# Kernel optimization log

Hardware: AMD Instinct MI355X
Metric: run time of the kernel (lower is better)

## Reference

```python
import jax, jax.numpy as jnp
import numpy as np
from jax import lax

SEQ, BATCH, D_IN, HID = 2048, 16, 512, 512


def _qrnn_dir(X, W, b):
    # X: [S, B, D]; W: [3H, D]; b: [3H]
    g = jnp.einsum('sbd,hd->sbh', X, W) + b            # [S, B, 3H]
    z, f, o = jnp.split(g, 3, axis=-1)
    z = jnp.tanh(z)
    f = jax.nn.sigmoid(f)
    o = jax.nn.sigmoid(o)
    # fo-pooling recurrence: h_t = f_t*z_t + (1-f_t)*h_{t-1}, h_0 = 0
    # linear recurrence h_t = a_t*h_{t-1} + c_t with a = 1-f, c = f*z
    a = 1.0 - f
    c = f * z

    def combine(e1, e2):
        a1, c1 = e1
        a2, c2 = e2
        return (a1 * a2, a2 * c1 + c2)

    _, h = lax.associative_scan(combine, (a, c), axis=0)
    return o * h                                        # [S, B, H]


def setup_inputs() -> dict:
    key = jax.random.key(0)
    k = jax.random.split(key, 5)
    scale = 0.02
    return {
        'X': jax.random.normal(k[0], (SEQ, BATCH, D_IN), dtype=jnp.float32),
        'W_fw': jax.random.normal(k[1], (3 * HID, D_IN), dtype=jnp.float32) * scale,
        'b_fw': jnp.zeros((3 * HID,), dtype=jnp.float32),
        'W_bw': jax.random.normal(k[2], (3 * HID, D_IN), dtype=jnp.float32) * scale,
        'b_bw': jnp.zeros((3 * HID,), dtype=jnp.float32),
    }


def reference(X, W_fw, b_fw, W_bw, b_bw):
    Yfw = _qrnn_dir(X, W_fw, b_fw)                       # [S, B, H]
    Ybw = _qrnn_dir(jnp.flip(X, axis=0), W_bw, b_bw)     # [S, B, H]
    return jnp.concatenate((Yfw, jnp.flip(Ybw, axis=0)), axis=2)  # [S, B, 2H]
```

## Files before the change

kernel.cpp:

```cpp
#include <hip/hip_runtime.h>
#include <hip/hip_bf16.h>

#define SEQ   2048
#define BATCH 16
#define DIN   512
#define HID   512
#define MROWS (SEQ*BATCH)
#define NCOLS (6*HID)
#define KDIM  DIN

#define NC   64
#define CL   32
#define NSEQ (2*BATCH*HID)

typedef unsigned short u16;
typedef __bf16 bf16x8 __attribute__((ext_vector_type(8)));
typedef float  f32x4  __attribute__((ext_vector_type(4)));

__device__ __forceinline__ u16 f2bf(float x) {
  unsigned u = __float_as_uint(x);
  unsigned r = (u + 0x7fffu + ((u >> 16) & 1u)) >> 16;
  return (u16)r;
}
__device__ __forceinline__ float bflo(unsigned u) { return __uint_as_float(u << 16); }
__device__ __forceinline__ float bfhi(unsigned u) { return __uint_as_float(u & 0xffff0000u); }

__device__ __forceinline__ void async_ld16(const void* g, void* l) {
  __builtin_amdgcn_global_load_lds(
      (const __attribute__((address_space(1))) void*)g,
      (__attribute__((address_space(3))) void*)l, 16, 0, 0);
}

__device__ __forceinline__ float sig_fast(float x) {
  return __builtin_amdgcn_rcpf(1.f + __expf(-x));
}
__device__ __forceinline__ float tanh_fast(float x) {
  return 1.f - 2.f * __builtin_amdgcn_rcpf(1.f + __expf(2.f * x));
}

__global__ void cvt_kernel(const float* __restrict__ in, u16* __restrict__ out, int n4) {
  int i = blockIdx.x * blockDim.x + threadIdx.x;
  if (i >= n4) return;
  const float4 v = ((const float4*)in)[i];
  uint2 r;
  r.x = (unsigned)f2bf(v.x) | ((unsigned)f2bf(v.y) << 16);
  r.y = (unsigned)f2bf(v.z) | ((unsigned)f2bf(v.w) << 16);
  ((uint2*)out)[i] = r;
}

__launch_bounds__(256)
__global__ void gemm_gates(const u16* __restrict__ A, const u16* __restrict__ B,
                           const float* __restrict__ bfw, const float* __restrict__ bbw,
                           u16* __restrict__ G)
{
  __shared__ u16 sA[128 * 64];
  __shared__ u16 sB[128 * 64];

  const int t    = threadIdx.x;
  const int wave = t >> 6;
  const int lane = t & 63;
  const int m0 = blockIdx.y * 128;
  const int n0 = blockIdx.x * 128;
  const int wm = (wave >> 1) * 64;
  const int wn = (wave & 1) * 64;

  f32x4 acc[4][4] = {};

  const int rloc = lane >> 3;
  const int gch  = (lane & 7) ^ rloc;
  const u16* gA = A + (size_t)(m0 + wave * 32 + rloc) * KDIM + gch * 8;
  const u16* gB = B + (size_t)(n0 + wave * 32 + rloc) * KDIM + gch * 8;

  const int lm  = lane & 15;
  const int q   = lane >> 4;
  const int xs  = lm & 7;

  for (int kt = 0; kt < KDIM; kt += 64) {
    __syncthreads();
#pragma unroll
    for (int j = 0; j < 4; j++) {
      async_ld16(gA + kt + (size_t)(j * 8) * KDIM, sA + (wave * 32 + j * 8) * 64);
      async_ld16(gB + kt + (size_t)(j * 8) * KDIM, sB + (wave * 32 + j * 8) * 64);
    }
    __syncthreads();

#pragma unroll
    for (int s = 0; s < 2; s++) {
      const int cofs = ((s * 4 + q) ^ xs) * 8;
      bf16x8 af[4], bfr[4];
#pragma unroll
      for (int mi = 0; mi < 4; mi++)
        af[mi] = *(const bf16x8*)(sA + (wm + mi * 16 + lm) * 64 + cofs);
#pragma unroll
      for (int ni = 0; ni < 4; ni++)
        bfr[ni] = *(const bf16x8*)(sB + (wn + ni * 16 + lm) * 64 + cofs);
#pragma unroll
      for (int mi = 0; mi < 4; mi++)
#pragma unroll
        for (int ni = 0; ni < 4; ni++)
          acc[mi][ni] = __builtin_amdgcn_mfma_f32_16x16x32_bf16(bfr[ni], af[mi], acc[mi][ni], 0, 0, 0);
    }
  }

  const int q4 = q * 4;
#pragma unroll
  for (int ni = 0; ni < 4; ni++) {
    const int colb = n0 + wn + ni * 16 + q4;
    const int dir  = colb >= 1536 ? 1 : 0;
    const int rem  = colb - dir * 1536;
    const int gate = rem >> 9;
    const int hb   = rem & 511;
    const float4 bias4 = *(const float4*)((dir ? bbw : bfw) + rem);
    u16* Gs = G + (size_t)(dir * 3 + gate) * MROWS * HID + hb;
#pragma unroll
    for (int mi = 0; mi < 4; mi++) {
      const int m = m0 + wm + mi * 16 + lm;
      float v0 = acc[mi][ni][0] + bias4.x;
      float v1 = acc[mi][ni][1] + bias4.y;
      float v2 = acc[mi][ni][2] + bias4.z;
      float v3 = acc[mi][ni][3] + bias4.w;
      if (gate == 0) {
        v0 = tanh_fast(v0); v1 = tanh_fast(v1); v2 = tanh_fast(v2); v3 = tanh_fast(v3);
      } else {
        v0 = sig_fast(v0); v1 = sig_fast(v1); v2 = sig_fast(v2); v3 = sig_fast(v3);
      }
      uint2 pk;
      pk.x = (unsigned)f2bf(v0) | ((unsigned)f2bf(v1) << 16);
      pk.y = (unsigned)f2bf(v2) | ((unsigned)f2bf(v3) << 16);
      *(uint2*)(Gs + (size_t)m * HID) = pk;
    }
  }
}

__global__ void scan_stage1(const u16* __restrict__ G, float* __restrict__ AC) {
  const int tid = blockIdx.x * 256 + threadIdx.x;
  const int h     = (tid & 127) * 4;
  const int chunk = (tid >> 7) & 63;
  const int b     = (tid >> 13) & 15;
  const int dir   = tid >> 17;
  const u16* Zp = G + (size_t)(dir * 3 + 0) * MROWS * HID;
  const u16* Fp = G + (size_t)(dir * 3 + 1) * MROWS * HID;
  float A0 = 1.f, A1 = 1.f, A2 = 1.f, A3 = 1.f;
  float C0 = 0.f, C1 = 0.f, C2 = 0.f, C3 = 0.f;
  const int tbase = chunk * CL;
#pragma unroll 8
  for (int i = 0; i < CL; i++) {
    const int ts = tbase + i;
    const int s = dir ? (SEQ - 1 - ts) : ts;
    const size_t off = ((size_t)s * BATCH + b) * HID + h;
    const uint2 zu = *(const uint2*)(Zp + off);
    const uint2 fu = *(const uint2*)(Fp + off);
    const float z0 = bflo(zu.x), z1 = bfhi(zu.x), z2 = bflo(zu.y), z3 = bfhi(zu.y);
    const float f0 = bflo(fu.x), f1 = bfhi(fu.x), f2 = bflo(fu.y), f3 = bfhi(fu.y);
    const float a0 = 1.f - f0, a1 = 1.f - f1, a2 = 1.f - f2, a3 = 1.f - f3;
    C0 = fmaf(a0, C0, f0 * z0); A0 *= a0;
    C1 = fmaf(a1, C1, f1 * z1); A1 *= a1;
    C2 = fmaf(a2, C2, f2 * z2); A2 *= a2;
    C3 = fmaf(a3, C3, f3 * z3); A3 *= a3;
  }
  const int sidx = (dir * BATCH + b) * HID + h;
  *(float4*)&AC[(size_t)chunk * (2 * NSEQ) + sidx]        = make_float4(A0, A1, A2, A3);
  *(float4*)&AC[(size_t)chunk * (2 * NSEQ) + NSEQ + sidx] = make_float4(C0, C1, C2, C3);
}

__global__ void scan_stage2(const float* __restrict__ AC, float* __restrict__ Hin) {
  const int sidx = blockIdx.x * 256 + threadIdx.x;
  float carry = 0.f;
  for (int chunk = 0; chunk < NC; chunk++) {
    Hin[(size_t)chunk * NSEQ + sidx] = carry;
    const float Aa = AC[(size_t)chunk * (2 * NSEQ) + sidx];
    const float Cc = AC[(size_t)chunk * (2 * NSEQ) + NSEQ + sidx];
    carry = fmaf(Aa, carry, Cc);
  }
}

__global__ void scan_stage3(const u16* __restrict__ G, const float* __restrict__ Hin,
                            float* __restrict__ out) {
  const int tid = blockIdx.x * 256 + threadIdx.x;
  const int h     = (tid & 127) * 4;
  const int chunk = (tid >> 7) & 63;
  const int b     = (tid >> 13) & 15;
  const int dir   = tid >> 17;
  const u16* Zp = G + (size_t)(dir * 3 + 0) * MROWS * HID;
  const u16* Fp = G + (size_t)(dir * 3 + 1) * MROWS * HID;
  const u16* Op = G + (size_t)(dir * 3 + 2) * MROWS * HID;
  const int sidx = (dir * BATCH + b) * HID + h;
  float4 hv = *(const float4*)&Hin[(size_t)chunk * NSEQ + sidx];
  const int tbase = chunk * CL;
#pragma unroll 8
  for (int i = 0; i < CL; i++) {
    const int ts = tbase + i;
    const int s = dir ? (SEQ - 1 - ts) : ts;
    const size_t off = ((size_t)s * BATCH + b) * HID + h;
    const uint2 zu = *(const uint2*)(Zp + off);
    const uint2 fu = *(const uint2*)(Fp + off);
    const uint2 ou = *(const uint2*)(Op + off);
    const float z0 = bflo(zu.x), z1 = bfhi(zu.x), z2 = bflo(zu.y), z3 = bfhi(zu.y);
    const float f0 = bflo(fu.x), f1 = bfhi(fu.x), f2 = bflo(fu.y), f3 = bfhi(fu.y);
    hv.x = fmaf(f0, z0 - hv.x, hv.x);
    hv.y = fmaf(f1, z1 - hv.y, hv.y);
    hv.z = fmaf(f2, z2 - hv.z, hv.z);
    hv.w = fmaf(f3, z3 - hv.w, hv.w);
    f32x4 ov;
    ov[0] = bflo(ou.x) * hv.x;
    ov[1] = bfhi(ou.x) * hv.y;
    ov[2] = bflo(ou.y) * hv.z;
    ov[3] = bfhi(ou.y) * hv.w;
    __builtin_nontemporal_store(ov,
        (f32x4*)&out[((size_t)s * BATCH + b) * (2 * HID) + (size_t)dir * HID + h]);
  }
}

extern "C" void kernel_launch(void* const* d_in, const int* in_sizes, int n_in,
                              void* d_out, int out_size, void* d_ws, size_t ws_size,
                              hipStream_t stream) {
  const float* X   = (const float*)d_in[0];
  const float* Wfw = (const float*)d_in[1];
  const float* bfw = (const float*)d_in[2];
  const float* Wbw = (const float*)d_in[3];
  const float* bbw = (const float*)d_in[4];
  float* out = (float*)d_out;

  char* ws = (char*)d_ws;
  u16*   Xb  = (u16*)ws;
  u16*   Wb  = (u16*)(ws + (size_t)MROWS * KDIM * 2);
  u16*   G   = (u16*)(ws + (size_t)MROWS * KDIM * 2 + (size_t)NCOLS * KDIM * 2);
  float* AC  = (float*)((char*)G + (size_t)6 * MROWS * HID * 2);
  float* Hin = (float*)((char*)AC + (size_t)NC * 2 * NSEQ * 4);

  cvt_kernel<<<(MROWS * KDIM / 4) / 256, 256, 0, stream>>>(X, Xb, MROWS * KDIM / 4);
  cvt_kernel<<<(3 * HID * KDIM / 4) / 256, 256, 0, stream>>>(Wfw, Wb, 3 * HID * KDIM / 4);
  cvt_kernel<<<(3 * HID * KDIM / 4) / 256, 256, 0, stream>>>(Wbw, Wb + (size_t)3 * HID * KDIM,
                                                             3 * HID * KDIM / 4);

  dim3 gg(NCOLS / 128, MROWS / 128);
  gemm_gates<<<gg, 256, 0, stream>>>(Xb, Wb, bfw, bbw, G);

  scan_stage1<<<(NSEQ * NC / 4) / 256, 256, 0, stream>>>(G, AC);
  scan_stage2<<<NSEQ / 256, 256, 0, stream>>>(AC, Hin);
  scan_stage3<<<(NSEQ * NC / 4) / 256, 256, 0, stream>>>(G, Hin, out);
}
```

Measured before the change: 402.2 us.

## Fuse gate activations and intra-chunk scan into GEMM epilogue

The GEMM tile now covers the z, f and o columns for one hidden slice and one direction, so each block can apply the activations and run a local chunked linear scan over its 128 rows in registers. Partial results cross between waves through LDS. The epilogue writes compact U = o*h_local and V = o*prod(a) arrays in fp16 plus per-chunk carry data. This drops the separate stage-1 scan pass and the six-gate bf16 intermediate. The output pass becomes a single FMA per element using the combined carry. The trade-off is a longer sequential carry combine over 256 chunks, a heavier GEMM epilogue with more accumulator registers, and fp16 storage whose range and precision may differ from the reference.

```diff
diff --git a/kernel.cpp b/kernel.cpp
--- a/kernel.cpp
+++ b/kernel.cpp
@@ -1,16 +1,15 @@
 #include <hip/hip_runtime.h>
 #include <hip/hip_bf16.h>
+#include <hip/hip_fp16.h>
 
 #define SEQ   2048
 #define BATCH 16
 #define DIN   512
 #define HID   512
 #define MROWS (SEQ*BATCH)
-#define NCOLS (6*HID)
 #define KDIM  DIN
 
-#define NC   64
-#define CL   32
+#define NCH  256
 #define NSEQ (2*BATCH*HID)
 
 typedef unsigned short u16;
@@ -22,8 +21,15 @@
   unsigned r = (u + 0x7fffu + ((u >> 16) & 1u)) >> 16;
   return (u16)r;
 }
-__device__ __forceinline__ float bflo(unsigned u) { return __uint_as_float(u << 16); }
-__device__ __forceinline__ float bfhi(unsigned u) { return __uint_as_float(u & 0xffff0000u); }
+
+__device__ __forceinline__ unsigned pkh(float a, float b) {
+  __half2 h = __floats2half2_rn(a, b);
+  return *(const unsigned*)&h;
+}
+__device__ __forceinline__ float2 uph(unsigned x) {
+  __half2 h = *(const __half2*)&x;
+  return __half22float2(h);
+}
 
 __device__ __forceinline__ void async_ld16(const void* g, void* l) {
   __builtin_amdgcn_global_load_lds(
@@ -49,163 +55,208 @@
 }
 
 __launch_bounds__(256)
-__global__ void gemm_gates(const u16* __restrict__ A, const u16* __restrict__ B,
+__global__ void gemm_fused(const u16* __restrict__ A, const u16* __restrict__ B,
                            const float* __restrict__ bfw, const float* __restrict__ bbw,
-                           u16* __restrict__ G)
+                           u16* __restrict__ U, u16* __restrict__ V,
+                           float* __restrict__ ACn)
 {
-  __shared__ u16 sA[128 * 64];
-  __shared__ u16 sB[128 * 64];
+  __shared__ __align__(16) u16 sA[128 * 64];
+  __shared__ __align__(16) u16 sB[192 * 64];
 
   const int t    = threadIdx.x;
   const int wave = t >> 6;
   const int lane = t & 63;
-  const int m0 = blockIdx.y * 128;
-  const int n0 = blockIdx.x * 128;
-  const int wm = (wave >> 1) * 64;
-  const int wn = (wave & 1) * 64;
-
-  f32x4 acc[4][4] = {};
+  const int m0  = blockIdx.y * 128;
+  const int dir = blockIdx.x >> 3;
+  const int hb  = (blockIdx.x & 7) * 64;
+  const int wm  = (wave >> 1) * 64;
+  const int p   = wave & 1;
+  const int wn  = p * 96;
+
+  f32x4 acc[4][6] = {};
 
   const int rloc = lane >> 3;
   const int gch  = (lane & 7) ^ rloc;
-  const u16* gA = A + (size_t)(m0 + wave * 32 + rloc) * KDIM + gch * 8;
-  const u16* gB = B + (size_t)(n0 + wave * 32 + rloc) * KDIM + gch * 8;
-
-  const int lm  = lane & 15;
-  const int q   = lane >> 4;
-  const int xs  = lm & 7;
+  const u16* gA  = A + (size_t)(m0 + wave * 32 + rloc) * KDIM + gch * 8;
+  const u16* WbD = B + (size_t)dir * (3 * HID * KDIM);
+  unsigned gBo[6];
+#pragma unroll
+  for (int j = 0; j < 6; j++) {
+    const int nl = wave * 48 + j * 8 + rloc;
+    const int pp = nl >= 96 ? 1 : 0;
+    const int r  = nl - pp * 96;
+    const int wrow = (r >> 5) * HID + hb + pp * 32 + (r & 31);
+    gBo[j] = (unsigned)(wrow * KDIM + gch * 8);
+  }
+
+  const int lm = lane & 15;
+  const int q  = lane >> 4;
+  const int xs = lm & 7;
 
   for (int kt = 0; kt < KDIM; kt += 64) {
     __syncthreads();
 #pragma unroll
-    for (int j = 0; j < 4; j++) {
+    for (int j = 0; j < 4; j++)
       async_ld16(gA + kt + (size_t)(j * 8) * KDIM, sA + (wave * 32 + j * 8) * 64);
-      async_ld16(gB + kt + (size_t)(j * 8) * KDIM, sB + (wave * 32 + j * 8) * 64);
-    }
+#pragma unroll
+    for (int j = 0; j < 6; j++)
+      async_ld16(WbD + gBo[j] + kt, sB + (wave * 48 + j * 8) * 64);
     __syncthreads();
 
 #pragma unroll
     for (int s = 0; s < 2; s++) {
       const int cofs = ((s * 4 + q) ^ xs) * 8;
-      bf16x8 af[4], bfr[4];
+      bf16x8 af[4], bfr[6];
 #pragma unroll
       for (int mi = 0; mi < 4; mi++)
         af[mi] = *(const bf16x8*)(sA + (wm + mi * 16 + lm) * 64 + cofs);
 #pragma unroll
-      for (int ni = 0; ni < 4; ni++)
+      for (int ni = 0; ni < 6; ni++)
         bfr[ni] = *(const bf16x8*)(sB + (wn + ni * 16 + lm) * 64 + cofs);
 #pragma unroll
       for (int mi = 0; mi < 4; mi++)
 #pragma unroll
-        for (int ni = 0; ni < 4; ni++)
+        for (int ni = 0; ni < 6; ni++)
           acc[mi][ni] = __builtin_amdgcn_mfma_f32_16x16x32_bf16(bfr[ni], af[mi], acc[mi][ni], 0, 0, 0);
     }
   }
 
-  const int q4 = q * 4;
-#pragma unroll
-  for (int ni = 0; ni < 4; ni++) {
-    const int colb = n0 + wn + ni * 16 + q4;
-    const int dir  = colb >= 1536 ? 1 : 0;
-    const int rem  = colb - dir * 1536;
-    const int gate = rem >> 9;
-    const int hb   = rem & 511;
-    const float4 bias4 = *(const float4*)((dir ? bbw : bfw) + rem);
-    u16* Gs = G + (size_t)(dir * 3 + gate) * MROWS * HID + hb;
-#pragma unroll
-    for (int mi = 0; mi < 4; mi++) {
-      const int m = m0 + wm + mi * 16 + lm;
-      float v0 = acc[mi][ni][0] + bias4.x;
-      float v1 = acc[mi][ni][1] + bias4.y;
-      float v2 = acc[mi][ni][2] + bias4.z;
-      float v3 = acc[mi][ni][3] + bias4.w;
-      if (gate == 0) {
-        v0 = tanh_fast(v0); v1 = tanh_fast(v1); v2 = tanh_fast(v2); v3 = tanh_fast(v3);
-      } else {
-        v0 = sig_fast(v0); v1 = sig_fast(v1); v2 = sig_fast(v2); v3 = sig_fast(v3);
+  const float* bias = dir ? bbw : bfw;
+  const int hcol0 = hb + p * 32 + q * 4;
+
+  f32x4 bz[2], bff[2], bo[2];
+#pragma unroll
+  for (int j = 0; j < 2; j++) {
+    float4 t0 = *(const float4*)(bias + 0 * HID + hcol0 + j * 16);
+    float4 t1 = *(const float4*)(bias + 1 * HID + hcol0 + j * 16);
+    float4 t2 = *(const float4*)(bias + 2 * HID + hcol0 + j * 16);
+    bz[j][0] = t0.x; bz[j][1] = t0.y; bz[j][2] = t0.z; bz[j][3] = t0.w;
+    bff[j][0] = t1.x; bff[j][1] = t1.y; bff[j][2] = t1.z; bff[j][3] = t1.w;
+    bo[j][0] = t2.x; bo[j][1] = t2.y; bo[j][2] = t2.z; bo[j][3] = t2.w;
+  }
+
+#pragma unroll
+  for (int mi = 0; mi < 4; mi++)
+#pragma unroll
+    for (int j = 0; j < 2; j++)
+#pragma unroll
+      for (int e = 0; e < 4; e++) {
+        const float z = tanh_fast(acc[mi][j][e] + bz[j][e]);
+        const float f = sig_fast(acc[mi][2 + j][e] + bff[j][e]);
+        const float o = sig_fast(acc[mi][4 + j][e] + bo[j][e]);
+        acc[mi][j][e]     = f * z;
+        acc[mi][2 + j][e] = 1.f - f;
+        acc[mi][4 + j][e] = o;
       }
-      uint2 pk;
-      pk.x = (unsigned)f2bf(v0) | ((unsigned)f2bf(v1) << 16);
-      pk.y = (unsigned)f2bf(v2) | ((unsigned)f2bf(v3) << 16);
-      *(uint2*)(Gs + (size_t)m * HID) = pk;
-    }
-  }
-}
-
-__global__ void scan_stage1(const u16* __restrict__ G, float* __restrict__ AC) {
-  const int tid = blockIdx.x * 256 + threadIdx.x;
-  const int h     = (tid & 127) * 4;
-  const int chunk = (tid >> 7) & 63;
-  const int b     = (tid >> 13) & 15;
-  const int dir   = tid >> 17;
-  const u16* Zp = G + (size_t)(dir * 3 + 0) * MROWS * HID;
-  const u16* Fp = G + (size_t)(dir * 3 + 1) * MROWS * HID;
-  float A0 = 1.f, A1 = 1.f, A2 = 1.f, A3 = 1.f;
-  float C0 = 0.f, C1 = 0.f, C2 = 0.f, C3 = 0.f;
-  const int tbase = chunk * CL;
-#pragma unroll 8
-  for (int i = 0; i < CL; i++) {
-    const int ts = tbase + i;
-    const int s = dir ? (SEQ - 1 - ts) : ts;
-    const size_t off = ((size_t)s * BATCH + b) * HID + h;
-    const uint2 zu = *(const uint2*)(Zp + off);
-    const uint2 fu = *(const uint2*)(Fp + off);
-    const float z0 = bflo(zu.x), z1 = bfhi(zu.x), z2 = bflo(zu.y), z3 = bfhi(zu.y);
-    const float f0 = bflo(fu.x), f1 = bfhi(fu.x), f2 = bflo(fu.y), f3 = bfhi(fu.y);
-    const float a0 = 1.f - f0, a1 = 1.f - f1, a2 = 1.f - f2, a3 = 1.f - f3;
-    C0 = fmaf(a0, C0, f0 * z0); A0 *= a0;
-    C1 = fmaf(a1, C1, f1 * z1); A1 *= a1;
-    C2 = fmaf(a2, C2, f2 * z2); A2 *= a2;
-    C3 = fmaf(a3, C3, f3 * z3); A3 *= a3;
-  }
-  const int sidx = (dir * BATCH + b) * HID + h;
-  *(float4*)&AC[(size_t)chunk * (2 * NSEQ) + sidx]        = make_float4(A0, A1, A2, A3);
-  *(float4*)&AC[(size_t)chunk * (2 * NSEQ) + NSEQ + sidx] = make_float4(C0, C1, C2, C3);
-}
-
-__global__ void scan_stage2(const float* __restrict__ AC, float* __restrict__ Hin) {
+
+#define SCAN_STEP(MI) { f32x4 a_ = acc[MI][2 + j], c_ = acc[MI][j]; \
+    Hc = a_ * Hc + c_; Pc = a_ * Pc; acc[MI][j] = Hc; acc[MI][2 + j] = Pc; }
+  if (!dir) {
+#pragma unroll
+    for (int j = 0; j < 2; j++) {
+      f32x4 Hc = {0.f, 0.f, 0.f, 0.f}, Pc = {1.f, 1.f, 1.f, 1.f};
+      SCAN_STEP(0) SCAN_STEP(1) SCAN_STEP(2) SCAN_STEP(3)
+    }
+  } else {
+#pragma unroll
+    for (int j = 0; j < 2; j++) {
+      f32x4 Hc = {0.f, 0.f, 0.f, 0.f}, Pc = {1.f, 1.f, 1.f, 1.f};
+      SCAN_STEP(3) SCAN_STEP(2) SCAN_STEP(1) SCAN_STEP(0)
+    }
+  }
+#undef SCAN_STEP
+
+  __syncthreads();
+  f32x4* ex = (f32x4*)sA;
+  const int slot = p * 64 + lane;
+  const bool firstHalf = ((wave >> 1) == (dir ? 1 : 0));
+  if (firstHalf) {
+#pragma unroll
+    for (int j = 0; j < 2; j++) {
+      f32x4 Pl = dir ? acc[0][2 + j] : acc[3][2 + j];
+      f32x4 Hl = dir ? acc[0][j]     : acc[3][j];
+      ex[slot * 4 + j * 2 + 0] = Pl;
+      ex[slot * 4 + j * 2 + 1] = Hl;
+    }
+  }
+  __syncthreads();
+  if (!firstHalf) {
+#pragma unroll
+    for (int j = 0; j < 2; j++) {
+      const f32x4 P0 = ex[slot * 4 + j * 2 + 0];
+      const f32x4 H0 = ex[slot * 4 + j * 2 + 1];
+#pragma unroll
+      for (int mi = 0; mi < 4; mi++) {
+        acc[mi][j]     = acc[mi][j] + acc[mi][2 + j] * H0;
+        acc[mi][2 + j] = acc[mi][2 + j] * P0;
+      }
+    }
+  }
+
+  const size_t mrowbase = ((size_t)dir * MROWS + (size_t)(m0 + wm + lm)) * HID + hcol0;
+#pragma unroll
+  for (int mi = 0; mi < 4; mi++) {
+    u16* Urow = U + mrowbase + (size_t)mi * 16 * HID;
+    u16* Vrow = V + mrowbase + (size_t)mi * 16 * HID;
+#pragma unroll
+    for (int j = 0; j < 2; j++) {
+      const f32x4 u = acc[mi][4 + j] * acc[mi][j];
+      const f32x4 v = acc[mi][4 + j] * acc[mi][2 + j];
+      uint2 up, vp;
+      up.x = pkh(u[0], u[1]); up.y = pkh(u[2], u[3]);
+      vp.x = pkh(v[0], v[1]); vp.y = pkh(v[2], v[3]);
+      *(uint2*)(Urow + j * 16) = up;
+      *(uint2*)(Vrow + j * 16) = vp;
+    }
+  }
+
+  if (!firstHalf) {
+    const int ct = dir ? (NCH - 1 - (int)blockIdx.y) : (int)blockIdx.y;
+    float* ACc = ACn + (size_t)ct * (2 * NSEQ) + (size_t)(dir * 16 + lm) * 512 + hcol0;
+#pragma unroll
+    for (int j = 0; j < 2; j++) {
+      const f32x4 Pf = dir ? acc[0][2 + j] : acc[3][2 + j];
+      const f32x4 Hf = dir ? acc[0][j]     : acc[3][j];
+      *(f32x4*)(ACc + j * 16)        = Pf;
+      *(f32x4*)(ACc + NSEQ + j * 16) = Hf;
+    }
+  }
+}
+
+__global__ void scan_combine(const float* __restrict__ ACn, float* __restrict__ Hin) {
   const int sidx = blockIdx.x * 256 + threadIdx.x;
   float carry = 0.f;
-  for (int chunk = 0; chunk < NC; chunk++) {
-    Hin[(size_t)chunk * NSEQ + sidx] = carry;
-    const float Aa = AC[(size_t)chunk * (2 * NSEQ) + sidx];
-    const float Cc = AC[(size_t)chunk * (2 * NSEQ) + NSEQ + sidx];
+  for (int ct = 0; ct < NCH; ct++) {
+    Hin[(size_t)ct * NSEQ + sidx] = carry;
+    const float Aa = ACn[(size_t)ct * (2 * NSEQ) + sidx];
+    const float Cc = ACn[(size_t)ct * (2 * NSEQ) + NSEQ + sidx];
     carry = fmaf(Aa, carry, Cc);
   }
 }
 
-__global__ void scan_stage3(const u16* __restrict__ G, const float* __restrict__ Hin,
-                            float* __restrict__ out) {
+__global__ void scan_out(const u16* __restrict__ U, const u16* __restrict__ V,
+                         const float* __restrict__ Hin, float* __restrict__ out) {
   const int tid = blockIdx.x * 256 + threadIdx.x;
-  const int h     = (tid & 127) * 4;
-  const int chunk = (tid >> 7) & 63;
-  const int b     = (tid >> 13) & 15;
-  const int dir   = tid >> 17;
-  const u16* Zp = G + (size_t)(dir * 3 + 0) * MROWS * HID;
-  const u16* Fp = G + (size_t)(dir * 3 + 1) * MROWS * HID;
-  const u16* Op = G + (size_t)(dir * 3 + 2) * MROWS * HID;
+  const int h   = (tid & 127) * 4;
+  const int ct  = (tid >> 7) & 255;
+  const int b   = (tid >> 15) & 15;
+  const int dir = tid >> 19;
   const int sidx = (dir * BATCH + b) * HID + h;
-  float4 hv = *(const float4*)&Hin[(size_t)chunk * NSEQ + sidx];
-  const int tbase = chunk * CL;
-#pragma unroll 8
-  for (int i = 0; i < CL; i++) {
-    const int ts = tbase + i;
-    const int s = dir ? (SEQ - 1 - ts) : ts;
-    const size_t off = ((size_t)s * BATCH + b) * HID + h;
-    const uint2 zu = *(const uint2*)(Zp + off);
-    const uint2 fu = *(const uint2*)(Fp + off);
-    const uint2 ou = *(const uint2*)(Op + off);
-    const float z0 = bflo(zu.x), z1 = bfhi(zu.x), z2 = bflo(zu.y), z3 = bfhi(zu.y);
-    const float f0 = bflo(fu.x), f1 = bfhi(fu.x), f2 = bflo(fu.y), f3 = bfhi(fu.y);
-    hv.x = fmaf(f0, z0 - hv.x, hv.x);
-    hv.y = fmaf(f1, z1 - hv.y, hv.y);
-    hv.z = fmaf(f2, z2 - hv.z, hv.z);
-    hv.w = fmaf(f3, z3 - hv.w, hv.w);
+  const float4 hv = *(const float4*)&Hin[(size_t)ct * NSEQ + sidx];
+#pragma unroll
+  for (int i = 0; i < 8; i++) {
+    const int ts = ct * 8 + i;
+    const int s  = dir ? (SEQ - 1 - ts) : ts;
+    const size_t off = ((size_t)dir * MROWS + (size_t)s * BATCH + b) * HID + h;
+    const uint2 uu = *(const uint2*)(U + off);
+    const uint2 vv = *(const uint2*)(V + off);
+    const float2 u01 = uph(uu.x), u23 = uph(uu.y);
+    const float2 v01 = uph(vv.x), v23 = uph(vv.y);
     f32x4 ov;
-    ov[0] = bflo(ou.x) * hv.x;
-    ov[1] = bfhi(ou.x) * hv.y;
-    ov[2] = bflo(ou.y) * hv.z;
-    ov[3] = bfhi(ou.y) * hv.w;
+    ov[0] = fmaf(v01.x, hv.x, u01.x);
+    ov[1] = fmaf(v01.y, hv.y, u01.y);
+    ov[2] = fmaf(v23.x, hv.z, u23.x);
+    ov[3] = fmaf(v23.y, hv.w, u23.y);
     __builtin_nontemporal_store(ov,
         (f32x4*)&out[((size_t)s * BATCH + b) * (2 * HID) + (size_t)dir * HID + h]);
   }
@@ -222,21 +273,25 @@
   float* out = (float*)d_out;
 
   char* ws = (char*)d_ws;
+  const size_t XB  = (size_t)MROWS * KDIM * 2;
+  const size_t WB  = (size_t)2 * 3 * HID * KDIM * 2;
+  const size_t UVB = (size_t)2 * MROWS * HID * 2;
   u16*   Xb  = (u16*)ws;
-  u16*   Wb  = (u16*)(ws + (size_t)MROWS * KDIM * 2);
-  u16*   G   = (u16*)(ws + (size_t)MROWS * KDIM * 2 + (size_t)NCOLS * KDIM * 2);
-  float* AC  = (float*)((char*)G + (size_t)6 * MROWS * HID * 2);
-  float* Hin = (float*)((char*)AC + (size_t)NC * 2 * NSEQ * 4);
+  u16*   Wb  = (u16*)(ws + XB);
+  u16*   U   = (u16*)(ws + XB + WB);
+  u16*   V   = (u16*)(ws + XB + WB + UVB);
+  float* ACn = (float*)(ws + XB + WB + 2 * UVB);
+  float* Hin = ACn + (size_t)NCH * 2 * NSEQ;
 
   cvt_kernel<<<(MROWS * KDIM / 4) / 256, 256, 0, stream>>>(X, Xb, MROWS * KDIM / 4);
   cvt_kernel<<<(3 * HID * KDIM / 4) / 256, 256, 0, stream>>>(Wfw, Wb, 3 * HID * KDIM / 4);
   cvt_kernel<<<(3 * HID * KDIM / 4) / 256, 256, 0, stream>>>(Wbw, Wb + (size_t)3 * HID * KDIM,
                                                              3 * HID * KDIM / 4);
 
-  dim3 gg(NCOLS / 128, MROWS / 128);
-  gemm_gates<<<gg, 256, 0, stream>>>(Xb, Wb, bfw, bbw, G);
-
-  scan_stage1<<<(NSEQ * NC / 4) / 256, 256, 0, stream>>>(G, AC);
-  scan_stage2<<<NSEQ / 256, 256, 0, stream>>>(AC, Hin);
-  scan_stage3<<<(NSEQ * NC / 4) / 256, 256, 0, stream>>>(G, Hin, out);
-}
+  dim3 gg(16, 256);
+  gemm_fused<<<gg, 256, 0, stream>>>(Xb, Wb, bfw, bbw, U, V, ACn);
+
+  scan_combine<<<NSEQ / 256, 256, 0, stream>>>(ACn, Hin);
+
+  scan_out<<<(2 * BATCH * NCH * 128) / 256, 256, 0, stream>>>(U, V, Hin, out);
+}
```

New measurement: 496.4 us. 1.23x slower.
